# Kernel optimization log

Hardware: AMD Instinct MI355X
Metric: run time of the kernel (lower is better)

Reference implementation:

```python
import jax, jax.numpy as jnp
import numpy as np

DIM = 768
NUM_HEADS = 12
MLP_RATIO = 4.0
HIDDEN = int(DIM * MLP_RATIO)
EPS = 1e-6  # flax LayerNorm default


def setup_inputs() -> dict:
    key = jax.random.key(0)
    ks = jax.random.split(key, 8)
    d = DIM
    init = lambda k, shape, fan_in: jax.random.normal(k, shape, jnp.float32) * (fan_in ** -0.5)
    return {
        "x": jax.random.normal(ks[0], (8, 1024, d), jnp.float32),
        "ln1_scale": jnp.ones((d,), jnp.float32),
        "ln1_bias": jnp.zeros((d,), jnp.float32),
        "qkv_w": init(ks[1], (d, 3 * d), d),
        "qkv_b": jnp.zeros((3 * d,), jnp.float32),
        "proj_w": init(ks[2], (d, d), d),
        "proj_b": jnp.zeros((d,), jnp.float32),
        "ln2_scale": jnp.ones((d,), jnp.float32),
        "ln2_bias": jnp.zeros((d,), jnp.float32),
        "fc1_w": init(ks[3], (d, HIDDEN), d),
        "fc1_b": jnp.zeros((HIDDEN,), jnp.float32),
        "fc2_w": init(ks[4], (HIDDEN, d), HIDDEN),
        "fc2_b": jnp.zeros((d,), jnp.float32),
    }


def _layernorm(x, scale, bias):
    mu = jnp.mean(x, axis=-1, keepdims=True)
    var = jnp.mean(jnp.square(x - mu), axis=-1, keepdims=True)
    return (x - mu) * jax.lax.rsqrt(var + EPS) * scale + bias


def reference(x, ln1_scale, ln1_bias, qkv_w, qkv_b, proj_w, proj_b,
              ln2_scale, ln2_bias, fc1_w, fc1_b, fc2_w, fc2_b):
    b, n, d = x.shape
    h = NUM_HEADS
    hd = d // h
    scale = hd ** -0.5

    # --- attention (pre-norm) ---
    y = _layernorm(x, ln1_scale, ln1_bias)
    qkv = y @ qkv_w + qkv_b                      # [b, n, 3d]
    qkv = qkv.reshape(b, n, 3, h, hd).transpose(2, 0, 3, 1, 4)  # [3, b, h, n, hd]
    q, k, v = qkv[0], qkv[1], qkv[2]
    attn = jnp.einsum("bhqd,bhkd->bhqk", q, k) * scale
    attn = jax.nn.softmax(attn, axis=-1)
    o = jnp.einsum("bhqk,bhkd->bhqd", attn, v)   # [b, h, n, hd]
    o = o.transpose(0, 2, 1, 3).reshape(b, n, d)
    x = x + (o @ proj_w + proj_b)

    # --- MLP (pre-norm) ---
    y = _layernorm(x, ln2_scale, ln2_bias)
    y = jax.nn.gelu(y @ fc1_w + fc1_b)
    x = x + (y @ fc2_w + fc2_b)
    return x
```

## Files before the change

### kernel.cpp

```cpp
#include <hip/hip_runtime.h>
#include <hip/hip_bf16.h>
#include <math.h>


#define DIM 768
#define SEQ 1024
#define BATCH 8
#define NHEAD 12
#define HDIM 64
#define HID 3072
#define MTOK (BATCH * SEQ)

typedef __attribute__((ext_vector_type(8))) short short8;
typedef __attribute__((ext_vector_type(4))) short short4v;
typedef __attribute__((ext_vector_type(4))) float floatx4;

__device__ __forceinline__ short f2s(float x) {
  __hip_bfloat16 h = __float2bfloat16(x);
  return __builtin_bit_cast(short, h);
}
__device__ __forceinline__ float s2f(short s) {
  return __bfloat162float(__builtin_bit_cast(__hip_bfloat16, s));
}
__device__ __forceinline__ floatx4 zf4() {
  floatx4 v; v[0] = v[1] = v[2] = v[3] = 0.f; return v;
}
__device__ __forceinline__ float gelu_f(float x) {
  float z = 0.7978845608028654f * (x + 0.044715f * x * x * x);
  float u = __expf(2.f * z);
  return 0.5f * x * (2.f - 2.f / (u + 1.f));
}

__global__ __launch_bounds__(256) void tr4_kernel(
    const float* __restrict__ w0, short* __restrict__ o0,
    const float* __restrict__ w1, short* __restrict__ o1,
    const float* __restrict__ w2, short* __restrict__ o2,
    const float* __restrict__ w3, short* __restrict__ o3) {
  __shared__ float tile[32][33];
  const int id = blockIdx.x;
  const float* in;
  short* out;
  int K, N, tid;
  if (id < 1728)      { in = w0; out = o0; K = DIM; N = 3 * DIM; tid = id; }
  else if (id < 2304) { in = w1; out = o1; K = DIM; N = DIM;     tid = id - 1728; }
  else if (id < 4608) { in = w2; out = o2; K = DIM; N = HID;     tid = id - 2304; }
  else                { in = w3; out = o3; K = HID; N = DIM;     tid = id - 4608; }
  const int ntx = N >> 5;
  const int n0 = (tid % ntx) * 32, k0 = (tid / ntx) * 32;
  const int tx = threadIdx.x & 31, ty = threadIdx.x >> 5;
#pragma unroll
  for (int i = 0; i < 4; ++i)
    tile[ty + i * 8][tx] = in[(size_t)(k0 + ty + i * 8) * N + n0 + tx];
  __syncthreads();
#pragma unroll
  for (int i = 0; i < 4; ++i)
    out[(size_t)(n0 + ty + i * 8) * K + k0 + tx] = f2s(tile[tx][ty + i * 8]);
}

__global__ __launch_bounds__(256) void ln_kernel(const float* __restrict__ x,
                                                 const float* __restrict__ scale,
                                                 const float* __restrict__ bias,
                                                 short* __restrict__ y) {
  const int row = blockIdx.x;
  const int t = threadIdx.x;
  const float* xr = x + (size_t)row * DIM;
  float v[3];
  float s1 = 0.f, s2 = 0.f;
#pragma unroll
  for (int j = 0; j < 3; ++j) {
    v[j] = xr[t + j * 256];
    s1 += v[j];
    s2 += v[j] * v[j];
  }
#pragma unroll
  for (int off = 32; off; off >>= 1) {
    s1 += __shfl_down(s1, off, 64);
    s2 += __shfl_down(s2, off, 64);
  }
  __shared__ float r1[4], r2[4], bc[2];
  const int wave = t >> 6, lane = t & 63;
  if (lane == 0) { r1[wave] = s1; r2[wave] = s2; }
  __syncthreads();
  if (t == 0) {
    float S1 = r1[0] + r1[1] + r1[2] + r1[3];
    float S2 = r2[0] + r2[1] + r2[2] + r2[3];
    float mu = S1 * (1.0f / DIM);
    float var = S2 * (1.0f / DIM) - mu * mu;
    bc[0] = mu;
    bc[1] = rsqrtf(fmaxf(var, 0.f) + 1e-6f);
  }
  __syncthreads();
  const float mu = bc[0], rstd = bc[1];
#pragma unroll
  for (int j = 0; j < 3; ++j) {
    const int idx = t + j * 256;
    y[(size_t)row * DIM + idx] = f2s((v[j] - mu) * rstd * scale[idx] + bias[idx]);
  }
}

template <int ROWS, int THREADS>
__device__ __forceinline__ void stageT(const short* __restrict__ src, int ld,
                                       short* lds, int t) {
#pragma unroll
  for (int i = 0; i < (ROWS * 4) / THREADS; ++i) {
    const int S = i * THREADS + t;
    const int row = S >> 2;
    const int chunk = (S & 3) ^ ((row >> 1) & 3);
    const short* g = src + (size_t)row * ld + chunk * 8;
    const unsigned off = __builtin_amdgcn_readfirstlane((unsigned)((S & ~63) * 16));
    __builtin_amdgcn_global_load_lds(
        (const __attribute__((address_space(1))) void*)g,
        (__attribute__((address_space(3))) void*)((char*)lds + off), 16, 0, 0);
  }
}

template <int ROWS, int THREADS>
__device__ __forceinline__ void stage8(const short* __restrict__ src, int ld,
                                       short* lds, int t) {
#pragma unroll
  for (int i = 0; i < (ROWS * 8) / THREADS; ++i) {
    const int S = i * THREADS + t;
    const int row = S >> 3;
    const int chunk = (S & 7) ^ (row & 7);
    const short* g = src + (size_t)row * ld + chunk * 8;
    const unsigned off = __builtin_amdgcn_readfirstlane((unsigned)((S & ~63) * 16));
    __builtin_amdgcn_global_load_lds(
        (const __attribute__((address_space(1))) void*)g,
        (__attribute__((address_space(3))) void*)((char*)lds + off), 16, 0, 0);
  }
}

template <int MODE>
__global__ __launch_bounds__(256) void gemm_mfma(
    const short* __restrict__ A, const short* __restrict__ Bt,
    const float* __restrict__ bias,
    short* __restrict__ outB,
    short* __restrict__ Qb, short* __restrict__ Kb, short* __restrict__ Vtb,
    int N, int K) {
  __shared__ __align__(16) short Asm[2][4096];
  __shared__ __align__(16) short Bsm[2][4096];
  const int t = threadIdx.x;
  const int lane = t & 63, w = t >> 6, quad = lane >> 4, l15 = lane & 15;

  const int nbx = gridDim.x;
  const int lid = blockIdx.y * nbx + blockIdx.x;
  const int xcd = lid & 7, local = lid >> 3;
  const int m0 = ((local / nbx) * 8 + xcd) * 128;
  const int n0 = (local % nbx) * 128;
  const int mb = (w & 1) * 64, nb = (w >> 1) * 64;

  floatx4 acc[4][4];
#pragma unroll
  for (int mi = 0; mi < 4; ++mi)
#pragma unroll
    for (int ni = 0; ni < 4; ++ni) acc[mi][ni] = zf4();

  stageT<128, 256>(A + (size_t)m0 * K, K, Asm[0], t);
  stageT<128, 256>(Bt + (size_t)n0 * K, K, Bsm[0], t);

  const int nk = K >> 5;
  for (int kt = 0; kt < nk; ++kt) {
    __syncthreads();
    const int cur = kt & 1;
    if (kt + 1 < nk) {
      stageT<128, 256>(A + (size_t)m0 * K + (kt + 1) * 32, K, Asm[cur ^ 1], t);
      stageT<128, 256>(Bt + (size_t)n0 * K + (kt + 1) * 32, K, Bsm[cur ^ 1], t);
    }
    short8 a[4], b[4];
#pragma unroll
    for (int mi = 0; mi < 4; ++mi) {
      const int r = mb + mi * 16 + l15;
      a[mi] = *(const short8*)(Asm[cur] + r * 32 + (quad ^ ((r >> 1) & 3)) * 8);
    }
#pragma unroll
    for (int ni = 0; ni < 4; ++ni) {
      const int r = nb + ni * 16 + l15;
      b[ni] = *(const short8*)(Bsm[cur] + r * 32 + (quad ^ ((r >> 1) & 3)) * 8);
    }
#pragma unroll
    for (int mi = 0; mi < 4; ++mi)
#pragma unroll
      for (int ni = 0; ni < 4; ++ni)
        acc[mi][ni] = __builtin_amdgcn_mfma_f32_16x16x32_bf16(a[mi], b[ni], acc[mi][ni], 0, 0, 0);
  }

#pragma unroll
  for (int mi = 0; mi < 4; ++mi) {
    const int row0 = m0 + mb + mi * 16 + quad * 4;
#pragma unroll
    for (int ni = 0; ni < 4; ++ni) {
      const int col = n0 + nb + ni * 16 + l15;
      const float bv = bias[col];
      float v[4];
#pragma unroll
      for (int r = 0; r < 4; ++r) v[r] = acc[mi][ni][r] + bv;
      if (MODE == 0) {
        const int bb = row0 >> 10;
        const int s0 = row0 & 1023;
        if (col < 1536) {
          const int cc = (col < 768) ? col : col - 768;
          const int h = cc >> 6, d = cc & 63;
          short* dst = (col < 768 ? Qb : Kb) + (size_t)(bb * NHEAD + h) * SEQ * HDIM;
#pragma unroll
          for (int r = 0; r < 4; ++r) dst[(size_t)(s0 + r) * HDIM + d] = f2s(v[r]);
        } else {
          const int cc = col - 1536;
          const int h = cc >> 6, d = cc & 63;
          short4v pv;
#pragma unroll
          for (int r = 0; r < 4; ++r) pv[r] = f2s(v[r]);
          *(short4v*)(Vtb + ((size_t)(bb * NHEAD + h) * HDIM + d) * SEQ + s0) = pv;
        }
      } else {
#pragma unroll
        for (int r = 0; r < 4; ++r)
          outB[(size_t)(row0 + r) * N + col] = f2s(gelu_f(v[r]));
      }
    }
  }
}

__global__ __launch_bounds__(128) void gemm_n64(
    const short* __restrict__ A, const short* __restrict__ Bt,
    const float* __restrict__ bias, const float* __restrict__ res,
    float* __restrict__ outF, int N, int K) {
  __shared__ __align__(16) short Asm[2][8192];
  __shared__ __align__(16) short Bsm[2][4096];
  const int t = threadIdx.x;
  const int lane = t & 63, w = t >> 6, quad = lane >> 4, l15 = lane & 15;

  const int nbx = gridDim.x;
  const int lid = blockIdx.y * nbx + blockIdx.x;
  const int xcd = lid & 7, local = lid >> 3;
  const int m0 = ((local / nbx) * 8 + xcd) * 128;
  const int n0 = (local % nbx) * 64;
  const int mb = w * 64;

  floatx4 acc[4][4];
#pragma unroll
  for (int mi = 0; mi < 4; ++mi)
#pragma unroll
    for (int ni = 0; ni < 4; ++ni) acc[mi][ni] = zf4();

  stage8<128, 128>(A + (size_t)m0 * K, K, Asm[0], t);
  stage8<64, 128>(Bt + (size_t)n0 * K, K, Bsm[0], t);

  const int nk = K >> 6;
  for (int kt = 0; kt < nk; ++kt) {
    __syncthreads();
    const int cur = kt & 1;
    if (kt + 1 < nk) {
      stage8<128, 128>(A + (size_t)m0 * K + (kt + 1) * 64, K, Asm[cur ^ 1], t);
      stage8<64, 128>(Bt + (size_t)n0 * K + (kt + 1) * 64, K, Bsm[cur ^ 1], t);
    }
#pragma unroll
    for (int ks = 0; ks < 2; ++ks) {
      short8 a[4], b[4];
#pragma unroll
      for (int mi = 0; mi < 4; ++mi) {
        const int r = mb + mi * 16 + l15;
        a[mi] = *(const short8*)(Asm[cur] + r * 64 + (((ks * 4 + quad) ^ (r & 7)) * 8));
      }
#pragma unroll
      for (int ni = 0; ni < 4; ++ni) {
        const int r = ni * 16 + l15;
        b[ni] = *(const short8*)(Bsm[cur] + r * 64 + (((ks * 4 + quad) ^ (r & 7)) * 8));
      }
#pragma unroll
      for (int mi = 0; mi < 4; ++mi)
#pragma unroll
        for (int ni = 0; ni < 4; ++ni)
          acc[mi][ni] = __builtin_amdgcn_mfma_f32_16x16x32_bf16(a[mi], b[ni], acc[mi][ni], 0, 0, 0);
    }
  }

#pragma unroll
  for (int mi = 0; mi < 4; ++mi) {
    const int row0 = m0 + mb + mi * 16 + quad * 4;
#pragma unroll
    for (int ni = 0; ni < 4; ++ni) {
      const int col = n0 + ni * 16 + l15;
      const float bv = bias[col];
#pragma unroll
      for (int r = 0; r < 4; ++r) {
        const size_t idx = (size_t)(row0 + r) * N + col;
        outF[idx] = acc[mi][ni][r] + bv + res[idx];
      }
    }
  }
}

__device__ __forceinline__ void stage64(const short* __restrict__ src, int ld,
                                        short* lds, int t) {
  const int lane = t & 63, w = t >> 6;
#pragma unroll
  for (int i = 0; i < 2; ++i) {
    const int S = w * 128 + i * 64 + lane;
    const int r = S >> 3, c0 = S & 7;
    const int c = c0 ^ (r & 7);
    const short* g = src + (size_t)r * ld + c * 8;
    const unsigned off = __builtin_amdgcn_readfirstlane((unsigned)((w * 128 + i * 64) * 16));
    __builtin_amdgcn_global_load_lds(
        (const __attribute__((address_space(1))) void*)g,
        (__attribute__((address_space(3))) void*)((char*)lds + off), 16, 0, 0);
  }
}

__global__ __launch_bounds__(256) void attn_kernel(
    const short* __restrict__ Qb, const short* __restrict__ Kb,
    const short* __restrict__ Vtb, short* __restrict__ o) {
  __shared__ __align__(16) short Ks[2][4096];
  __shared__ __align__(16) short Vts[2][4096];
  __shared__ __align__(16) short Pt[8192];
  const int t = threadIdx.x;
  const int lane = t & 63, w = t >> 6, quad = lane >> 4, l15 = lane & 15;
  const int q0 = blockIdx.x * 128;
  const int bh = blockIdx.y;
  const size_t qkbase = (size_t)bh * SEQ * HDIM;
  const size_t vbase = (size_t)bh * HDIM * SEQ;
  short* ptw = Pt + w * 2048;

  short8 bq[2][2];
#pragma unroll
  for (int mi = 0; mi < 2; ++mi)
#pragma unroll
    for (int ks = 0; ks < 2; ++ks)
      bq[mi][ks] = *(const short8*)(Qb + qkbase +
                                    (size_t)(q0 + w * 32 + mi * 16 + l15) * HDIM +
                                    ks * 32 + quad * 8);

  floatx4 oacc[4][2];
  float m_st[2], l_st[2];
#pragma unroll
  for (int mi = 0; mi < 2; ++mi) { m_st[mi] = -1e30f; l_st[mi] = 0.f; }
#pragma unroll
  for (int di = 0; di < 4; ++di)
#pragma unroll
    for (int mi = 0; mi < 2; ++mi) oacc[di][mi] = zf4();

  stage64(Kb + qkbase, HDIM, Ks[0], t);
  stage64(Vtb + vbase, SEQ, Vts[0], t);

  for (int kt = 0; kt < 16; ++kt) {
    __syncthreads();
    const int cur = kt & 1;
    if (kt < 15) {
      stage64(Kb + qkbase + (size_t)(kt + 1) * 64 * HDIM, HDIM, Ks[cur ^ 1], t);
      stage64(Vtb + vbase + (kt + 1) * 64, SEQ, Vts[cur ^ 1], t);
    }

    floatx4 sacc[4][2];
#pragma unroll
    for (int ni = 0; ni < 4; ++ni)
#pragma unroll
      for (int mi = 0; mi < 2; ++mi) sacc[ni][mi] = zf4();
#pragma unroll
    for (int ks = 0; ks < 2; ++ks) {
      short8 ak[4];
#pragma unroll
      for (int ni = 0; ni < 4; ++ni) {
        const int r = ni * 16 + l15;
        ak[ni] = *(const short8*)(Ks[cur] + r * 64 + (((ks * 4 + quad) ^ (r & 7)) * 8));
      }
#pragma unroll
      for (int ni = 0; ni < 4; ++ni)
#pragma unroll
        for (int mi = 0; mi < 2; ++mi)
          sacc[ni][mi] = __builtin_amdgcn_mfma_f32_16x16x32_bf16(ak[ni], bq[mi][ks], sacc[ni][mi], 0, 0, 0);
    }

    float alpha[2];
#pragma unroll
    for (int mi = 0; mi < 2; ++mi) {
      float mx = -1e30f;
#pragma unroll
      for (int ni = 0; ni < 4; ++ni)
#pragma unroll
        for (int r = 0; r < 4; ++r) mx = fmaxf(mx, sacc[ni][mi][r]);
      mx = fmaxf(mx, __shfl_xor(mx, 16, 64));
      mx = fmaxf(mx, __shfl_xor(mx, 32, 64));
      mx *= 0.125f;
      const float mn = fmaxf(m_st[mi], mx);
      alpha[mi] = __expf(m_st[mi] - mn);
      m_st[mi] = mn;
      float rs = 0.f;
      const int row = mi * 16 + l15;
      const int swz = (row & 7) ^ ((row & 8) >> 1);
#pragma unroll
      for (int ni = 0; ni < 4; ++ni) {
        short4v pk;
#pragma unroll
        for (int r = 0; r < 4; ++r) {
          const float p = __expf(sacc[ni][mi][r] * 0.125f - mn);
          rs += p;
          pk[r] = f2s(p);
        }
        const int c = ni * 2 + (quad >> 1);
        *(short4v*)(ptw + row * 64 + ((c ^ swz) * 8 + (quad & 1) * 4)) = pk;
      }
      rs += __shfl_xor(rs, 16, 64);
      rs += __shfl_xor(rs, 32, 64);
      l_st[mi] = l_st[mi] * alpha[mi] + rs;
    }
#pragma unroll
    for (int di = 0; di < 4; ++di)
#pragma unroll
      for (int mi = 0; mi < 2; ++mi)
#pragma unroll
        for (int r = 0; r < 4; ++r) oacc[di][mi][r] *= alpha[mi];

#pragma unroll
    for (int ks = 0; ks < 2; ++ks) {
      short8 bp[2];
#pragma unroll
      for (int mi = 0; mi < 2; ++mi) {
        const int row = mi * 16 + l15;
        const int swz = (row & 7) ^ ((row & 8) >> 1);
        bp[mi] = *(const short8*)(ptw + row * 64 + (((ks * 4 + quad) ^ swz) * 8));
      }
      short8 av[4];
#pragma unroll
      for (int di = 0; di < 4; ++di) {
        const int r = di * 16 + l15;
        av[di] = *(const short8*)(Vts[cur] + r * 64 + (((ks * 4 + quad) ^ (r & 7)) * 8));
      }
#pragma unroll
      for (int di = 0; di < 4; ++di)
#pragma unroll
        for (int mi = 0; mi < 2; ++mi)
          oacc[di][mi] = __builtin_amdgcn_mfma_f32_16x16x32_bf16(av[di], bp[mi], oacc[di][mi], 0, 0, 0);
    }
  }

  const int bb = bh / NHEAD, hh = bh % NHEAD;
  float inv[2];
#pragma unroll
  for (int mi = 0; mi < 2; ++mi) inv[mi] = 1.0f / l_st[mi];
#pragma unroll
  for (int di = 0; di < 4; ++di)
#pragma unroll
    for (int mi = 0; mi < 2; ++mi) {
      const int tok = bb * SEQ + q0 + w * 32 + mi * 16 + l15;
      const int d = hh * HDIM + di * 16 + quad * 4;
      short4v ov;
#pragma unroll
      for (int r = 0; r < 4; ++r) ov[r] = f2s(oacc[di][mi][r] * inv[mi]);
      *(short4v*)(o + (size_t)tok * DIM + d) = ov;
    }
}

extern "C" void kernel_launch(void* const* d_in, const int* in_sizes, int n_in,
                              void* d_out, int out_size, void* d_ws, size_t ws_size,
                              hipStream_t stream) {
  const float* x      = (const float*)d_in[0];
  const float* ln1_s  = (const float*)d_in[1];
  const float* ln1_b  = (const float*)d_in[2];
  const float* qkv_w  = (const float*)d_in[3];
  const float* qkv_b  = (const float*)d_in[4];
  const float* proj_w = (const float*)d_in[5];
  const float* proj_b = (const float*)d_in[6];
  const float* ln2_s  = (const float*)d_in[7];
  const float* ln2_b  = (const float*)d_in[8];
  const float* fc1_w  = (const float*)d_in[9];
  const float* fc1_b  = (const float*)d_in[10];
  const float* fc2_w  = (const float*)d_in[11];
  const float* fc2_b  = (const float*)d_in[12];
  float* out = (float*)d_out;

  char* p = (char*)d_ws;
  short* wqt = (short*)p; p += (size_t)(3 * DIM) * DIM * 2;
  short* wpt = (short*)p; p += (size_t)DIM * DIM * 2;
  short* w1t = (short*)p; p += (size_t)HID * DIM * 2;
  short* w2t = (short*)p; p += (size_t)DIM * HID * 2;
  short* y   = (short*)p; p += (size_t)MTOK * DIM * 2;
  short* Qb  = (short*)p; p += (size_t)MTOK * DIM * 2;
  short* Kb  = (short*)p; p += (size_t)MTOK * DIM * 2;
  short* Vtb = (short*)p; p += (size_t)MTOK * DIM * 2;
  float* x1  = (float*)p; p += (size_t)MTOK * DIM * 4;
  short* h   = (short*)p; p += (size_t)MTOK * HID * 2;
  short* obuf = y;
  short* y2   = Qb;

  tr4_kernel<<<6912, 256, 0, stream>>>(qkv_w, wqt, proj_w, wpt, fc1_w, w1t, fc2_w, w2t);

  ln_kernel<<<MTOK, 256, 0, stream>>>(x, ln1_s, ln1_b, y);
  gemm_mfma<0><<<dim3(18, 64), 256, 0, stream>>>(
      y, wqt, qkv_b, nullptr, Qb, Kb, Vtb, 3 * DIM, DIM);
  attn_kernel<<<dim3(SEQ / 128, BATCH * NHEAD), 256, 0, stream>>>(Qb, Kb, Vtb, obuf);
  gemm_n64<<<dim3(12, 64), 128, 0, stream>>>(
      obuf, wpt, proj_b, x, x1, DIM, DIM);
  ln_kernel<<<MTOK, 256, 0, stream>>>(x1, ln2_s, ln2_b, y2);
  gemm_mfma<2><<<dim3(24, 64), 256, 0, stream>>>(
      y2, w1t, fc1_b, h, nullptr, nullptr, nullptr, HID, DIM);
  gemm_n64<<<dim3(12, 64), 128, 0, stream>>>(
      h, w2t, fc2_b, x1, out, DIM, HID);
}
```

Baseline: 373.9 us.

## Fuse weight transpose with first layernorm and enlarge GEMM tile to 256x128

```diff
diff --git a/kernel.cpp b/kernel.cpp
--- a/kernel.cpp
+++ b/kernel.cpp
@@ -31,30 +31,70 @@
   return 0.5f * x * (2.f - 2.f / (u + 1.f));
 }
 
-__global__ __launch_bounds__(256) void tr4_kernel(
+__global__ __launch_bounds__(256) void pre_kernel(
     const float* __restrict__ w0, short* __restrict__ o0,
     const float* __restrict__ w1, short* __restrict__ o1,
     const float* __restrict__ w2, short* __restrict__ o2,
-    const float* __restrict__ w3, short* __restrict__ o3) {
-  __shared__ float tile[32][33];
+    const float* __restrict__ w3, short* __restrict__ o3,
+    const float* __restrict__ x, const float* __restrict__ ls,
+    const float* __restrict__ lb, short* __restrict__ y) {
   const int id = blockIdx.x;
-  const float* in;
-  short* out;
-  int K, N, tid;
-  if (id < 1728)      { in = w0; out = o0; K = DIM; N = 3 * DIM; tid = id; }
-  else if (id < 2304) { in = w1; out = o1; K = DIM; N = DIM;     tid = id - 1728; }
-  else if (id < 4608) { in = w2; out = o2; K = DIM; N = HID;     tid = id - 2304; }
-  else                { in = w3; out = o3; K = HID; N = DIM;     tid = id - 4608; }
-  const int ntx = N >> 5;
-  const int n0 = (tid % ntx) * 32, k0 = (tid / ntx) * 32;
-  const int tx = threadIdx.x & 31, ty = threadIdx.x >> 5;
-#pragma unroll
-  for (int i = 0; i < 4; ++i)
-    tile[ty + i * 8][tx] = in[(size_t)(k0 + ty + i * 8) * N + n0 + tx];
-  __syncthreads();
-#pragma unroll
-  for (int i = 0; i < 4; ++i)
-    out[(size_t)(n0 + ty + i * 8) * K + k0 + tx] = f2s(tile[tx][ty + i * 8]);
+  const int t = threadIdx.x;
+  if (id < 6912) {
+    __shared__ float tile[32][33];
+    const float* in;
+    short* out;
+    int K, N, tid;
+    if (id < 1728)      { in = w0; out = o0; K = DIM; N = 3 * DIM; tid = id; }
+    else if (id < 2304) { in = w1; out = o1; K = DIM; N = DIM;     tid = id - 1728; }
+    else if (id < 4608) { in = w2; out = o2; K = DIM; N = HID;     tid = id - 2304; }
+    else                { in = w3; out = o3; K = HID; N = DIM;     tid = id - 4608; }
+    const int ntx = N >> 5;
+    const int n0 = (tid % ntx) * 32, k0 = (tid / ntx) * 32;
+    const int tx = t & 31, ty = t >> 5;
+#pragma unroll
+    for (int i = 0; i < 4; ++i)
+      tile[ty + i * 8][tx] = in[(size_t)(k0 + ty + i * 8) * N + n0 + tx];
+    __syncthreads();
+#pragma unroll
+    for (int i = 0; i < 4; ++i)
+      out[(size_t)(n0 + ty + i * 8) * K + k0 + tx] = f2s(tile[tx][ty + i * 8]);
+  } else {
+    const int row = id - 6912;
+    const float* xr = x + (size_t)row * DIM;
+    float v[3];
+    float s1 = 0.f, s2 = 0.f;
+#pragma unroll
+    for (int j = 0; j < 3; ++j) {
+      v[j] = xr[t + j * 256];
+      s1 += v[j];
+      s2 += v[j] * v[j];
+    }
+#pragma unroll
+    for (int off = 32; off; off >>= 1) {
+      s1 += __shfl_down(s1, off, 64);
+      s2 += __shfl_down(s2, off, 64);
+    }
+    __shared__ float r1[4], r2[4], bc[2];
+    const int wave = t >> 6, lane = t & 63;
+    if (lane == 0) { r1[wave] = s1; r2[wave] = s2; }
+    __syncthreads();
+    if (t == 0) {
+      float S1 = r1[0] + r1[1] + r1[2] + r1[3];
+      float S2 = r2[0] + r2[1] + r2[2] + r2[3];
+      float mu = S1 * (1.0f / DIM);
+      float var = S2 * (1.0f / DIM) - mu * mu;
+      bc[0] = mu;
+      bc[1] = rsqrtf(fmaxf(var, 0.f) + 1e-6f);
+    }
+    __syncthreads();
+    const float mu = bc[0], rstd = bc[1];
+#pragma unroll
+    for (int j = 0; j < 3; ++j) {
+      const int idx = t + j * 256;
+      y[(size_t)row * DIM + idx] = f2s((v[j] - mu) * rstd * ls[idx] + lb[idx]);
+    }
+  }
 }
 
 __global__ __launch_bounds__(256) void ln_kernel(const float* __restrict__ x,
@@ -131,13 +171,13 @@
 }
 
 template <int MODE>
-__global__ __launch_bounds__(256) void gemm_mfma(
+__global__ __launch_bounds__(512) void gemm_w512(
     const short* __restrict__ A, const short* __restrict__ Bt,
     const float* __restrict__ bias,
     short* __restrict__ outB,
     short* __restrict__ Qb, short* __restrict__ Kb, short* __restrict__ Vtb,
     int N, int K) {
-  __shared__ __align__(16) short Asm[2][4096];
+  __shared__ __align__(16) short Asm[2][8192];
   __shared__ __align__(16) short Bsm[2][4096];
   const int t = threadIdx.x;
   const int lane = t & 63, w = t >> 6, quad = lane >> 4, l15 = lane & 15;
@@ -145,9 +185,9 @@
   const int nbx = gridDim.x;
   const int lid = blockIdx.y * nbx + blockIdx.x;
   const int xcd = lid & 7, local = lid >> 3;
-  const int m0 = ((local / nbx) * 8 + xcd) * 128;
+  const int m0 = ((local / nbx) * 8 + xcd) * 256;
   const int n0 = (local % nbx) * 128;
-  const int mb = (w & 1) * 64, nb = (w >> 1) * 64;
+  const int mb = (w >> 1) * 64, nb = (w & 1) * 64;
 
   floatx4 acc[4][4];
 #pragma unroll
@@ -155,16 +195,16 @@
 #pragma unroll
     for (int ni = 0; ni < 4; ++ni) acc[mi][ni] = zf4();
 
-  stageT<128, 256>(A + (size_t)m0 * K, K, Asm[0], t);
-  stageT<128, 256>(Bt + (size_t)n0 * K, K, Bsm[0], t);
+  stageT<256, 512>(A + (size_t)m0 * K, K, Asm[0], t);
+  stageT<128, 512>(Bt + (size_t)n0 * K, K, Bsm[0], t);
 
   const int nk = K >> 5;
   for (int kt = 0; kt < nk; ++kt) {
     __syncthreads();
     const int cur = kt & 1;
     if (kt + 1 < nk) {
-      stageT<128, 256>(A + (size_t)m0 * K + (kt + 1) * 32, K, Asm[cur ^ 1], t);
-      stageT<128, 256>(Bt + (size_t)n0 * K + (kt + 1) * 32, K, Bsm[cur ^ 1], t);
+      stageT<256, 512>(A + (size_t)m0 * K + (kt + 1) * 32, K, Asm[cur ^ 1], t);
+      stageT<128, 512>(Bt + (size_t)n0 * K + (kt + 1) * 32, K, Bsm[cur ^ 1], t);
     }
     short8 a[4], b[4];
 #pragma unroll
@@ -481,16 +521,15 @@
   short* obuf = y;
   short* y2   = Qb;
 
-  tr4_kernel<<<6912, 256, 0, stream>>>(qkv_w, wqt, proj_w, wpt, fc1_w, w1t, fc2_w, w2t);
-
-  ln_kernel<<<MTOK, 256, 0, stream>>>(x, ln1_s, ln1_b, y);
-  gemm_mfma<0><<<dim3(18, 64), 256, 0, stream>>>(
+  pre_kernel<<<6912 + MTOK, 256, 0, stream>>>(qkv_w, wqt, proj_w, wpt, fc1_w, w1t,
+                                              fc2_w, w2t, x, ln1_s, ln1_b, y);
+  gemm_w512<0><<<dim3(18, 32), 512, 0, stream>>>(
       y, wqt, qkv_b, nullptr, Qb, Kb, Vtb, 3 * DIM, DIM);
   attn_kernel<<<dim3(SEQ / 128, BATCH * NHEAD), 256, 0, stream>>>(Qb, Kb, Vtb, obuf);
   gemm_n64<<<dim3(12, 64), 128, 0, stream>>>(
       obuf, wpt, proj_b, x, x1, DIM, DIM);
   ln_kernel<<<MTOK, 256, 0, stream>>>(x1, ln2_s, ln2_b, y2);
-  gemm_mfma<2><<<dim3(24, 64), 256, 0, stream>>>(
+  gemm_w512<2><<<dim3(24, 32), 512, 0, stream>>>(
       y2, w1t, fc1_b, h, nullptr, nullptr, nullptr, HID, DIM);
   gemm_n64<<<dim3(12, 64), 128, 0, stream>>>(
       h, w2t, fc2_b, x1, out, DIM, HID);
```

New measurement: 371.1 us. Within noise of the previous version (-0.7%).
